# Kernel optimization log

Measured on AMD Instinct MI355X. Metric: run time of the kernel, lower is better.

Reference implementation:

```python
import jax, jax.numpy as jnp
import numpy as np

K = 3  # kernel_size

def setup_inputs() -> dict:
    key = jax.random.key(0)
    k1, k2, k3 = jax.random.split(key, 3)
    B, C, H, W = 8, 64, 128, 128
    x = jax.random.normal(k1, (B, C, H, W), dtype=jnp.float32)
    # 1x1 conv weight (out_channels*K*K, in_channels) and bias
    W_gen = jax.random.normal(k2, (C * K * K, C), dtype=jnp.float32) / np.float32(np.sqrt(C))
    b_gen = jax.random.normal(k3, (C * K * K,), dtype=jnp.float32) * 0.01
    return {"x": x, "W_gen": W_gen, "b_gen": b_gen}

def reference(x, W_gen, b_gen):
    B, C, H, W = x.shape  # out_channels == in_channels (required by the view)
    # filter_gen: 1x1 conv + ReLU -> (B, C*K*K, H, W)
    f = jax.nn.relu(jnp.einsum('bchw,oc->bohw', x, W_gen) + b_gen[None, :, None, None])
    filters = f.reshape(B, C, K * K, H, W)
    # F.unfold with padding=(K-1)//2, stride 1: gather KxK patches per pixel.
    pad = (K - 1) // 2
    xp = jnp.pad(x, ((0, 0), (0, 0), (pad, pad), (pad, pad)))
    # kernel-position index runs row-major (i*K + j), matching unfold layout
    patches = jnp.stack([xp[:, :, i:i + H, j:j + W]
                         for i in range(K) for j in range(K)], axis=2)  # (B,C,K*K,H,W)
    out = (filters * patches).sum(axis=2)  # (B,C,H,W)
    return out
```

## Files before the change

### kernel.cpp

```cpp
#include <hip/hip_runtime.h>
#include <hip/hip_bf16.h>

#define CC 64
#define HH 128
#define WW 128
#define OO 576
#define HW (HH * WW)

typedef __attribute__((ext_vector_type(8))) short short8;
typedef __attribute__((ext_vector_type(4))) float floatx4;

__device__ __forceinline__ unsigned short f2bf(float f) {
    unsigned u = __float_as_uint(f);
    u = (u + 0x7FFFu + ((u >> 16) & 1u)) >> 16;
    return (unsigned short)u;
}

__global__ void ACDA_wconv_kernel(const float* __restrict__ Wg,
                                  unsigned short* __restrict__ Wb) {
    int i = blockIdx.x * 256 + threadIdx.x;
    if (i < OO * CC) Wb[i] = f2bf(Wg[i]);
}

__global__ __launch_bounds__(256) void ACDA_main_kernel(
    const float* __restrict__ x, const unsigned short* __restrict__ Wb,
    const float* __restrict__ bg, float* __restrict__ out)
{
    __shared__ __align__(16) char smem[20480];
    float (*FbufT)[64][20] = reinterpret_cast<float(*)[64][20]>(smem);
    unsigned short (*Bl)[72] = reinterpret_cast<unsigned short(*)[72]>(smem);

    const int tid  = threadIdx.x;
    const int lane = tid & 63;
    const int wv   = tid >> 6;
    const int quad = lane >> 4;
    const int l16  = lane & 15;

    const int bid = blockIdx.x;
    const int wk  = (bid & 7) * 256 + (bid >> 3);
    const int seg = wk & 1;
    const int h   = (wk >> 1) & 127;
    const int b   = wk >> 8;
    const int w0  = seg << 6;

    const float* xb = x + (size_t)b * CC * HW;

    int wA = w0 + lane - 1; bool badA = (wA < 0);   if (badA) wA = 0;
    int wB = w0 + lane;
    int wC = w0 + lane + 1; bool badC = (wC > 127); if (badC) wC = 127;
    int rt[3]; bool rbad[3];
#pragma unroll
    for (int di = 0; di < 3; ++di) {
        int rr = h + di - 1;
        rbad[di] = (rr < 0) || (rr > 127);
        rr = rr < 0 ? 0 : (rr > 127 ? 127 : rr);
        rt[di] = rr * WW;
    }
    const int wsel[3]  = {wA, wB, wC};
    const bool wbad[3] = {badA, false, badC};
    const int soffC = wv * 16 * HW;
    int  pb[3][3]; bool bad[3][3];
#pragma unroll
    for (int di = 0; di < 3; ++di)
#pragma unroll
        for (int dj = 0; dj < 3; ++dj) {
            pb[di][dj]  = soffC + rt[di] + wsel[dj];
            bad[di][dj] = rbad[di] || wbad[dj];
        }

    {
        const int w = w0 + lane;
#pragma unroll
        for (int cc = 0; cc < 16; cc += 2) {
            const int c = wv * 16 + cc;
            float f0 = xb[(c * HH + h) * WW + w];
            float f1 = xb[((c + 1) * HH + h) * WW + w];
            __hip_bfloat162 p = __float22bfloat162_rn(make_float2(f0, f1));
            unsigned u;
            __builtin_memcpy(&u, &p, 4);
            *(unsigned*)&Bl[lane][c] = u;
        }
    }

    float oacc[16];
#pragma unroll
    for (int i = 0; i < 16; ++i) oacc[i] = 0.f;

    short8 a0A, a1A, a0B, a1B;
    floatx4 bvA, bvB;
    float pvA[16], pvB[16];

#define LOADA(T, A0, A1, BV) do {                                         \
        const int obase_ = wv * 144 + (T) * 16;                           \
        const unsigned short* wrow_ = Wb + (obase_ + l16) * CC + quad * 8;\
        (A0) = *(const short8*)(wrow_);                                   \
        (A1) = *(const short8*)(wrow_ + 32);                              \
        (BV) = *(const floatx4*)(bg + obase_ + quad * 4);                 \
    } while (0)

#define LOADP(T, PV) do {                                                 \
        _Pragma("unroll")                                                 \
        for (int r_ = 0; r_ < 16; ++r_) {                                 \
            const int idx_ = (T) * 16 + r_;                               \
            const int c_   = idx_ / 9;                                    \
            const int kk_  = idx_ - 9 * c_;                               \
            const int di_  = kk_ / 3;                                     \
            const int dj_  = kk_ - 3 * di_;                               \
            float v_ = xb[pb[di_][dj_] + c_ * HW];                        \
            (PV)[r_] = bad[di_][dj_] ? 0.f : v_;                          \
        }                                                                 \
    } while (0)

    LOADA(0, a0A, a1A, bvA);
    LOADP(0, pvA);

    __syncthreads();

    short8 bfrag[4][2];
#pragma unroll
    for (int nt = 0; nt < 4; ++nt)
#pragma unroll
        for (int ks = 0; ks < 2; ++ks)
            bfrag[nt][ks] = *(const short8*)&Bl[nt * 16 + l16][ks * 32 + quad * 8];

    __syncthreads();

#define CHUNK(T, PVC, PVN, A0C, A1C, BVC, A0N, A1N, BVN) do {             \
        _Pragma("unroll")                                                 \
        for (int nt_ = 0; nt_ < 4; ++nt_) {                               \
            floatx4 z_ = (BVC);    \
            z_ = __builtin_amdgcn_mfma_f32_16x16x32_bf16((A0C), bfrag[nt_][0], z_, 0, 0, 0); \
            z_ = __builtin_amdgcn_mfma_f32_16x16x32_bf16((A1C), bfrag[nt_][1], z_, 0, 0, 0); \
            *(floatx4*)&FbufT[wv][nt_ * 16 + l16][quad * 4] = z_;         \
        }                                                                 \
        if ((T) < 8) {                                                    \
            LOADA((T) + 1, A0N, A1N, BVN);                                \
            LOADP((T) + 1, PVN);                                          \
        }                                                                 \
        _Pragma("unroll")                                                 \
        for (int g_ = 0; g_ < 4; ++g_) {                                  \
            floatx4 f4_ = *(const floatx4*)&FbufT[wv][lane][g_ * 4];      \
            _Pragma("unroll")                                             \
            for (int rr_ = 0; rr_ < 4; ++rr_) {                           \
                const int r_   = g_ * 4 + rr_;                            \
                const int idx_ = (T) * 16 + r_;                           \
                const int c_   = idx_ / 9;                                \
                float fv_ = fmaxf(f4_[rr_], 0.f);                         \
                oacc[c_] = fmaf(fv_, (PVC)[r_], oacc[c_]);                \
            }                                                             \
        }                                                                 \
    } while (0)

    CHUNK(0, pvA, pvB, a0A, a1A, bvA, a0B, a1B, bvB);
    CHUNK(1, pvB, pvA, a0B, a1B, bvB, a0A, a1A, bvA);
    CHUNK(2, pvA, pvB, a0A, a1A, bvA, a0B, a1B, bvB);
    CHUNK(3, pvB, pvA, a0B, a1B, bvB, a0A, a1A, bvA);
    CHUNK(4, pvA, pvB, a0A, a1A, bvA, a0B, a1B, bvB);
    CHUNK(5, pvB, pvA, a0B, a1B, bvB, a0A, a1A, bvA);
    CHUNK(6, pvA, pvB, a0A, a1A, bvA, a0B, a1B, bvB);
    CHUNK(7, pvB, pvA, a0B, a1B, bvB, a0A, a1A, bvA);
    CHUNK(8, pvA, pvB, a0A, a1A, bvA, a0B, a1B, bvB);

#undef CHUNK
#undef LOADP
#undef LOADA

    float* ob = out + (size_t)b * CC * HW + h * WW + w0 + lane;
#pragma unroll
    for (int i = 0; i < 16; ++i)
        ob[(wv * 16 + i) * HW] = oacc[i];
}

extern "C" void kernel_launch(void* const* d_in, const int* in_sizes, int n_in,
                              void* d_out, int out_size, void* d_ws, size_t ws_size,
                              hipStream_t stream) {
    const float* x  = (const float*)d_in[0];
    const float* Wg = (const float*)d_in[1];
    const float* bg = (const float*)d_in[2];
    float* out = (float*)d_out;
    unsigned short* Wb = (unsigned short*)d_ws;

    ACDA_wconv_kernel<<<dim3((OO * CC + 255) / 256), dim3(256), 0, stream>>>(Wg, Wb);
    ACDA_main_kernel<<<dim3(8 * 128 * 2), dim3(256), 0, stream>>>(x, Wb, bg, out);
}
```

Before: 112.3 us.

## Stage unfold patch loads directly into LDS with global_load_lds double buffering

Replaces register-held prefetch of the 16 patch values per chunk with direct global-to-LDS loads into a per-wave double buffer, and adds a launch bound hint of 4 blocks per SM. The aim is to free registers (pvA/pvB arrays) to raise occupancy while still overlapping patch fetches with MFMA work. It adds 32 KB of LDS per block, which can cap occupancy instead, and a full vmcnt(0) wait each chunk that may serialize the weight and patch prefetches.

```diff
diff --git a/kernel.cpp b/kernel.cpp
--- a/kernel.cpp
+++ b/kernel.cpp
@@ -22,13 +22,14 @@
     if (i < OO * CC) Wb[i] = f2bf(Wg[i]);
 }
 
-__global__ __launch_bounds__(256) void ACDA_main_kernel(
+__global__ __launch_bounds__(256, 4) void ACDA_main_kernel(
     const float* __restrict__ x, const unsigned short* __restrict__ Wb,
     const float* __restrict__ bg, float* __restrict__ out)
 {
     __shared__ __align__(16) char smem[20480];
     float (*FbufT)[64][20] = reinterpret_cast<float(*)[64][20]>(smem);
     unsigned short (*Bl)[72] = reinterpret_cast<unsigned short(*)[72]>(smem);
+    __shared__ float PLDS[4][2][16][64];
 
     const int tid  = threadIdx.x;
     const int lane = tid & 63;
@@ -68,6 +69,32 @@
             bad[di][dj] = rbad[di] || wbad[dj];
         }
 
+#define STAGEP(T, BUF) do {                                                   \
+        _Pragma("unroll")                                                     \
+        for (int r_ = 0; r_ < 16; ++r_) {                                     \
+            const int idx_ = (T) * 16 + r_;                                   \
+            const int c_   = idx_ / 9;                                        \
+            const int kk_  = idx_ - 9 * c_;                                   \
+            const int di_  = kk_ / 3;                                         \
+            const int dj_  = kk_ - 3 * di_;                                   \
+            const float* g_ = xb + pb[di_][dj_] + c_ * HW;                    \
+            __builtin_amdgcn_global_load_lds(                                 \
+                (const __attribute__((address_space(1))) unsigned int*)g_,    \
+                (__attribute__((address_space(3))) unsigned int*)&PLDS[wv][BUF][r_][0], \
+                4, 0, 0);                                                     \
+        }                                                                     \
+    } while (0)
+
+#define LOADA(T, A0, A1, BV) do {                                         \
+        const int obase_ = wv * 144 + (T) * 16;                           \
+        const unsigned short* wrow_ = Wb + (obase_ + l16) * CC + quad * 8;\
+        (A0) = *(const short8*)(wrow_);                                   \
+        (A1) = *(const short8*)(wrow_ + 32);                              \
+        (BV) = *(const floatx4*)(bg + obase_ + quad * 4);                 \
+    } while (0)
+
+    STAGEP(0, 0);
+
     {
         const int w = w0 + lane;
 #pragma unroll
@@ -88,31 +115,7 @@
 
     short8 a0A, a1A, a0B, a1B;
     floatx4 bvA, bvB;
-    float pvA[16], pvB[16];
-
-#define LOADA(T, A0, A1, BV) do {                                         \
-        const int obase_ = wv * 144 + (T) * 16;                           \
-        const unsigned short* wrow_ = Wb + (obase_ + l16) * CC + quad * 8;\
-        (A0) = *(const short8*)(wrow_);                                   \
-        (A1) = *(const short8*)(wrow_ + 32);                              \
-        (BV) = *(const floatx4*)(bg + obase_ + quad * 4);                 \
-    } while (0)
-
-#define LOADP(T, PV) do {                                                 \
-        _Pragma("unroll")                                                 \
-        for (int r_ = 0; r_ < 16; ++r_) {                                 \
-            const int idx_ = (T) * 16 + r_;                               \
-            const int c_   = idx_ / 9;                                    \
-            const int kk_  = idx_ - 9 * c_;                               \
-            const int di_  = kk_ / 3;                                     \
-            const int dj_  = kk_ - 3 * di_;                               \
-            float v_ = xb[pb[di_][dj_] + c_ * HW];                        \
-            (PV)[r_] = bad[di_][dj_] ? 0.f : v_;                          \
-        }                                                                 \
-    } while (0)
-
     LOADA(0, a0A, a1A, bvA);
-    LOADP(0, pvA);
 
     __syncthreads();
 
@@ -125,7 +128,7 @@
 
     __syncthreads();
 
-#define CHUNK(T, PVC, PVN, A0C, A1C, BVC, A0N, A1N, BVN) do {             \
+#define CHUNK(T, A0C, A1C, BVC, A0N, A1N, BVN) do {                       \
         _Pragma("unroll")                                                 \
         for (int nt_ = 0; nt_ < 4; ++nt_) {                               \
             floatx4 z_ = (BVC);    \
@@ -133,10 +136,8 @@
             z_ = __builtin_amdgcn_mfma_f32_16x16x32_bf16((A1C), bfrag[nt_][1], z_, 0, 0, 0); \
             *(floatx4*)&FbufT[wv][nt_ * 16 + l16][quad * 4] = z_;         \
         }                                                                 \
-        if ((T) < 8) {                                                    \
-            LOADA((T) + 1, A0N, A1N, BVN);                                \
-            LOADP((T) + 1, PVN);                                          \
-        }                                                                 \
+        if ((T) < 8) LOADA((T) + 1, A0N, A1N, BVN);                       \
+        asm volatile("s_waitcnt vmcnt(0)" ::: "memory");                  \
         _Pragma("unroll")                                                 \
         for (int g_ = 0; g_ < 4; ++g_) {                                  \
             floatx4 f4_ = *(const floatx4*)&FbufT[wv][lane][g_ * 4];      \
@@ -145,25 +146,31 @@
                 const int r_   = g_ * 4 + rr_;                            \
                 const int idx_ = (T) * 16 + r_;                           \
                 const int c_   = idx_ / 9;                                \
+                const int kk_  = idx_ - 9 * c_;                           \
+                const int di_  = kk_ / 3;                                 \
+                const int dj_  = kk_ - 3 * di_;                           \
                 float fv_ = fmaxf(f4_[rr_], 0.f);                         \
-                oacc[c_] = fmaf(fv_, (PVC)[r_], oacc[c_]);                \
+                float pv_ = PLDS[wv][(T) & 1][r_][lane];                  \
+                if (bad[di_][dj_]) pv_ = 0.f;                             \
+                oacc[c_] = fmaf(fv_, pv_, oacc[c_]);                      \
             }                                                             \
         }                                                                 \
+        if ((T) < 8) STAGEP((T) + 1, ((T) + 1) & 1);                      \
     } while (0)
 
-    CHUNK(0, pvA, pvB, a0A, a1A, bvA, a0B, a1B, bvB);
-    CHUNK(1, pvB, pvA, a0B, a1B, bvB, a0A, a1A, bvA);
-    CHUNK(2, pvA, pvB, a0A, a1A, bvA, a0B, a1B, bvB);
-    CHUNK(3, pvB, pvA, a0B, a1B, bvB, a0A, a1A, bvA);
-    CHUNK(4, pvA, pvB, a0A, a1A, bvA, a0B, a1B, bvB);
-    CHUNK(5, pvB, pvA, a0B, a1B, bvB, a0A, a1A, bvA);
-    CHUNK(6, pvA, pvB, a0A, a1A, bvA, a0B, a1B, bvB);
-    CHUNK(7, pvB, pvA, a0B, a1B, bvB, a0A, a1A, bvA);
-    CHUNK(8, pvA, pvB, a0A, a1A, bvA, a0B, a1B, bvB);
+    CHUNK(0, a0A, a1A, bvA, a0B, a1B, bvB);
+    CHUNK(1, a0B, a1B, bvB, a0A, a1A, bvA);
+    CHUNK(2, a0A, a1A, bvA, a0B, a1B, bvB);
+    CHUNK(3, a0B, a1B, bvB, a0A, a1A, bvA);
+    CHUNK(4, a0A, a1A, bvA, a0B, a1B, bvB);
+    CHUNK(5, a0B, a1B, bvB, a0A, a1A, bvA);
+    CHUNK(6, a0A, a1A, bvA, a0B, a1B, bvB);
+    CHUNK(7, a0B, a1B, bvB, a0A, a1A, bvA);
+    CHUNK(8, a0A, a1A, bvA, a0B, a1B, bvB);
 
 #undef CHUNK
-#undef LOADP
 #undef LOADA
+#undef STAGEP
 
     float* ob = out + (size_t)b * CC * HW + h * WW + w0 + lane;
 #pragma unroll
```

New measurement: 116.5 us. 3.8% more time.

## Reorder generated-filter rows by kernel position and loop over taps

Applied to the files above, without the earlier changes.

Permutes the bf16 weight matrix so each MFMA tile covers one kernel tap for 16 channels. Each output accumulator then receives a direct FMA instead of going through an index divide by 9. The nine unrolled chunks become a rolled loop over taps that loads the 16 patch values for the current tap only, rather than prefetching the next chunk's patches. It also sets a launch-bounds occupancy hint of 4 blocks per CU. The aim is lower register pressure and simpler addressing, at the cost of less overlap for patch loads and strided bias loads.

```diff
diff --git a/kernel.cpp b/kernel.cpp
--- a/kernel.cpp
+++ b/kernel.cpp
@@ -19,10 +19,16 @@
 __global__ void ACDA_wconv_kernel(const float* __restrict__ Wg,
                                   unsigned short* __restrict__ Wb) {
     int i = blockIdx.x * 256 + threadIdx.x;
-    if (i < OO * CC) Wb[i] = f2bf(Wg[i]);
+    if (i < OO * CC) {
+        int o2  = i >> 6;
+        int col = i & 63;
+        int kk  = o2 >> 6;
+        int c   = o2 & 63;
+        Wb[i] = f2bf(Wg[(c * 9 + kk) * CC + col]);
+    }
 }
 
-__global__ __launch_bounds__(256) void ACDA_main_kernel(
+__global__ __launch_bounds__(256, 4) void ACDA_main_kernel(
     const float* __restrict__ x, const unsigned short* __restrict__ Wb,
     const float* __restrict__ bg, float* __restrict__ out)
 {
@@ -35,6 +41,7 @@
     const int wv   = tid >> 6;
     const int quad = lane >> 4;
     const int l16  = lane & 15;
+    const int c0   = wv * 16;
 
     const int bid = blockIdx.x;
     const int wk  = (bid & 7) * 256 + (bid >> 3);
@@ -48,31 +55,13 @@
     int wA = w0 + lane - 1; bool badA = (wA < 0);   if (badA) wA = 0;
     int wB = w0 + lane;
     int wC = w0 + lane + 1; bool badC = (wC > 127); if (badC) wC = 127;
-    int rt[3]; bool rbad[3];
-#pragma unroll
-    for (int di = 0; di < 3; ++di) {
-        int rr = h + di - 1;
-        rbad[di] = (rr < 0) || (rr > 127);
-        rr = rr < 0 ? 0 : (rr > 127 ? 127 : rr);
-        rt[di] = rr * WW;
-    }
-    const int wsel[3]  = {wA, wB, wC};
-    const bool wbad[3] = {badA, false, badC};
-    const int soffC = wv * 16 * HW;
-    int  pb[3][3]; bool bad[3][3];
-#pragma unroll
-    for (int di = 0; di < 3; ++di)
-#pragma unroll
-        for (int dj = 0; dj < 3; ++dj) {
-            pb[di][dj]  = soffC + rt[di] + wsel[dj];
-            bad[di][dj] = rbad[di] || wbad[dj];
-        }
+    const int soffC = c0 * HW;
 
     {
         const int w = w0 + lane;
 #pragma unroll
         for (int cc = 0; cc < 16; cc += 2) {
-            const int c = wv * 16 + cc;
+            const int c = c0 + cc;
             float f0 = xb[(c * HH + h) * WW + w];
             float f1 = xb[((c + 1) * HH + h) * WW + w];
             __hip_bfloat162 p = __float22bfloat162_rn(make_float2(f0, f1));
@@ -88,31 +77,16 @@
 
     short8 a0A, a1A, a0B, a1B;
     floatx4 bvA, bvB;
-    float pvA[16], pvB[16];
-
-#define LOADA(T, A0, A1, BV) do {                                         \
-        const int obase_ = wv * 144 + (T) * 16;                           \
-        const unsigned short* wrow_ = Wb + (obase_ + l16) * CC + quad * 8;\
-        (A0) = *(const short8*)(wrow_);                                   \
-        (A1) = *(const short8*)(wrow_ + 32);                              \
-        (BV) = *(const floatx4*)(bg + obase_ + quad * 4);                 \
-    } while (0)
-
-#define LOADP(T, PV) do {                                                 \
-        _Pragma("unroll")                                                 \
-        for (int r_ = 0; r_ < 16; ++r_) {                                 \
-            const int idx_ = (T) * 16 + r_;                               \
-            const int c_   = idx_ / 9;                                    \
-            const int kk_  = idx_ - 9 * c_;                               \
-            const int di_  = kk_ / 3;                                     \
-            const int dj_  = kk_ - 3 * di_;                               \
-            float v_ = xb[pb[di_][dj_] + c_ * HW];                        \
-            (PV)[r_] = bad[di_][dj_] ? 0.f : v_;                          \
-        }                                                                 \
+#define LOADA(KK, A0, A1, BV) do {                                          \
+        const unsigned short* wrow_ = Wb + ((KK) * 64 + c0 + l16) * CC + quad * 8; \
+        (A0) = *(const short8*)(wrow_);                                     \
+        (A1) = *(const short8*)(wrow_ + 32);                                \
+        const float* bp_ = bg + (c0 + quad * 4) * 9 + (KK);                 \
+        (BV)[0] = bp_[0]; (BV)[1] = bp_[9];                                 \
+        (BV)[2] = bp_[18]; (BV)[3] = bp_[27];                               \
     } while (0)
 
     LOADA(0, a0A, a1A, bvA);
-    LOADP(0, pvA);
 
     __syncthreads();
 
@@ -125,50 +99,54 @@
 
     __syncthreads();
 
-#define CHUNK(T, PVC, PVN, A0C, A1C, BVC, A0N, A1N, BVN) do {             \
-        _Pragma("unroll")                                                 \
-        for (int nt_ = 0; nt_ < 4; ++nt_) {                               \
-            floatx4 z_ = (BVC);    \
+#define BODY(KK, A0C, A1C, BVC, A0N, A1N, BVN, PREF) do {                   \
+        if (PREF) LOADA((KK) + 1, A0N, A1N, BVN);                           \
+        const int di_ = (KK) < 3 ? 0 : ((KK) < 6 ? 1 : 2);                  \
+        const int dj_ = (KK) - 3 * di_;                                     \
+        int rr_ = h + di_ - 1;                                              \
+        const bool rbad_ = (rr_ < 0) || (rr_ > 127);                        \
+        rr_ = rr_ < 0 ? 0 : (rr_ > 127 ? 127 : rr_);                        \
+        const int  wsel_ = (dj_ == 0) ? wA : ((dj_ == 1) ? wB : wC);        \
+        const bool wbad_ = (dj_ == 0) ? badA : ((dj_ == 2) ? badC : false); \
+        const bool badk_ = rbad_ || wbad_;                                  \
+        const int  pbk_  = soffC + rr_ * WW + wsel_;                        \
+        float pv_[16];                                                      \
+        _Pragma("unroll")                                                   \
+        for (int r_ = 0; r_ < 16; ++r_) pv_[r_] = xb[pbk_ + r_ * HW];       \
+        _Pragma("unroll")                                                   \
+        for (int nt_ = 0; nt_ < 4; ++nt_) {                                 \
+            floatx4 z_ = (BVC);      \
             z_ = __builtin_amdgcn_mfma_f32_16x16x32_bf16((A0C), bfrag[nt_][0], z_, 0, 0, 0); \
             z_ = __builtin_amdgcn_mfma_f32_16x16x32_bf16((A1C), bfrag[nt_][1], z_, 0, 0, 0); \
-            *(floatx4*)&FbufT[wv][nt_ * 16 + l16][quad * 4] = z_;         \
-        }                                                                 \
-        if ((T) < 8) {                                                    \
-            LOADA((T) + 1, A0N, A1N, BVN);                                \
-            LOADP((T) + 1, PVN);                                          \
-        }                                                                 \
-        _Pragma("unroll")                                                 \
-        for (int g_ = 0; g_ < 4; ++g_) {                                  \
-            floatx4 f4_ = *(const floatx4*)&FbufT[wv][lane][g_ * 4];      \
-            _Pragma("unroll")                                             \
-            for (int rr_ = 0; rr_ < 4; ++rr_) {                           \
-                const int r_   = g_ * 4 + rr_;                            \
-                const int idx_ = (T) * 16 + r_;                           \
-                const int c_   = idx_ / 9;                                \
-                float fv_ = fmaxf(f4_[rr_], 0.f);                         \
-                oacc[c_] = fmaf(fv_, (PVC)[r_], oacc[c_]);                \
-            }                                                             \
-        }                                                                 \
+            *(floatx4*)&FbufT[wv][nt_ * 16 + l16][quad * 4] = z_;           \
+        }                                                                   \
+        _Pragma("unroll")                                                   \
+        for (int g_ = 0; g_ < 4; ++g_) {                                    \
+            floatx4 f4_ = *(const floatx4*)&FbufT[wv][lane][g_ * 4];        \
+            _Pragma("unroll")                                               \
+            for (int rr2_ = 0; rr2_ < 4; ++rr2_) {                          \
+                const int r_ = g_ * 4 + rr2_;                               \
+                float fv_ = fmaxf(f4_[rr2_], 0.f);                          \
+                float pvv_ = badk_ ? 0.f : pv_[r_];                         \
+                oacc[r_] = fmaf(fv_, pvv_, oacc[r_]);                       \
+            }                                                               \
+        }                                                                   \
     } while (0)
 
-    CHUNK(0, pvA, pvB, a0A, a1A, bvA, a0B, a1B, bvB);
-    CHUNK(1, pvB, pvA, a0B, a1B, bvB, a0A, a1A, bvA);
-    CHUNK(2, pvA, pvB, a0A, a1A, bvA, a0B, a1B, bvB);
-    CHUNK(3, pvB, pvA, a0B, a1B, bvB, a0A, a1A, bvA);
-    CHUNK(4, pvA, pvB, a0A, a1A, bvA, a0B, a1B, bvB);
-    CHUNK(5, pvB, pvA, a0B, a1B, bvB, a0A, a1A, bvA);
-    CHUNK(6, pvA, pvB, a0A, a1A, bvA, a0B, a1B, bvB);
-    CHUNK(7, pvB, pvA, a0B, a1B, bvB, a0A, a1A, bvA);
-    CHUNK(8, pvA, pvB, a0A, a1A, bvA, a0B, a1B, bvB);
+#pragma unroll 1
+    for (int kk = 0; kk < 8; kk += 2) {
+        BODY(kk,     a0A, a1A, bvA, a0B, a1B, bvB, true);
+        BODY(kk + 1, a0B, a1B, bvB, a0A, a1A, bvA, true);
+    }
+    BODY(8, a0A, a1A, bvA, a0B, a1B, bvB, false);
 
-#undef CHUNK
-#undef LOADP
+#undef BODY
 #undef LOADA
 
     float* ob = out + (size_t)b * CC * HW + h * WW + w0 + lane;
 #pragma unroll
     for (int i = 0; i < 16; ++i)
-        ob[(wv * 16 + i) * HW] = oacc[i];
+        ob[(c0 + i) * HW] = oacc[i];
 }
 
 extern "C" void kernel_launch(void* const* d_in, const int* in_sizes, int n_in,
```

Measured after the change: 113.6 us. No clear change (+1.1%).
